# Performance work log

Hardware: AMD Instinct MI355X
Metric: run time of the kernel (lower is better)

Reference implementation:

```python
import jax, jax.numpy as jnp
import numpy as np


def _knn_graph(x, k):
    """Faithful port of DynamicLstmGnn.knn_to_graph + get_u_v, returning the
    dense symmetrized edge-weight matrix [N, N] (the original re-sparsifies
    this same matrix via coalesce; nonzero extraction is data-dependent and
    not jit-able, so the dense matrix is the canonical output)."""
    N = x.shape[0]
    # negative squared euclidean distance: -||xi||^2 + 2 xi.xj - ||xj||^2
    xx = jnp.sum(x * x, axis=1, keepdims=True)          # [N, 1]
    inner = -2.0 * (x @ x.T)                              # [N, N]
    pairwise_distance = -xx - inner - xx.T                # [N, N], <= 0
    vals, idx = jax.lax.top_k(pairwise_distance, k)       # [N, k] largest (= closest)
    rows = jnp.repeat(jnp.arange(N), k)                   # idx_prime.flatten()
    # sparse COO -> to_dense (duplicate indices sum, matching torch.sparse)
    edges = jnp.zeros((N, N), dtype=x.dtype).at[rows, idx.ravel()].add(vals.ravel())
    edges_int = (edges > 0).astype(x.dtype)
    reflected_int = edges_int + edges_int.T
    reflected_edges = edges + edges.T
    denom = jnp.where(reflected_int == 0, jnp.ones((), x.dtype), reflected_int)
    edges = reflected_edges / denom
    diag = jnp.arange(N)
    edges = edges.at[diag, diag].set(0.0)                 # fill_diagonal_(0)
    return edges


def setup_inputs() -> dict:
    key = jax.random.key(0)
    x = jax.random.normal(key, (10000, 64), dtype=jnp.float32)
    return {"x": x, "k": 5}


def reference(x, k):
    return _knn_graph(x, k)
```

## Files before the change

kernel.cpp:

```cpp
#include <hip/hip_runtime.h>

#define D 64
#define K 5
#define LK 8
#define GK 12
#define NSPLIT 16
#define NTILES 625
#define ROWBLK 157
#define NCOMP (ROWBLK * NSPLIT)
typedef unsigned int u32;
typedef unsigned long long u64;
typedef __bf16 bf16x8 __attribute__((ext_vector_type(8)));
typedef float  f32x4v __attribute__((ext_vector_type(4)));

__device__ __forceinline__ u32 med3u(u32 a, u32 b, u32 c) {
    u32 r;
    asm("v_med3_u32 %0, %1, %2, %3" : "=v"(r) : "v"(a), "v"(b), "v"(c));
    return r;
}

__device__ __forceinline__ u32 pack32(float v, int idx) {
    u32 u = __float_as_uint(v);
    u ^= ((u32)((int)u >> 31)) | 0x80000000u;
    return (u & 0xFFFFC000u) | ((~(u32)idx) & 0x3FFFu);
}
__device__ __forceinline__ int idx32(u32 key) { return (int)((~key) & 0x3FFFu); }

__device__ __forceinline__ u64 packKV(float v, int idx) {
    u32 u = __float_as_uint(v);
    u ^= ((u32)((int)u >> 31)) | 0x80000000u;
    return ((u64)u << 32) | (u32)(~idx);
}
__device__ __forceinline__ float unpackV(u64 key) {
    u32 hu = (u32)(key >> 32);
    return (hu & 0x80000000u) ? __uint_as_float(hu & 0x7fffffffu)
                              : __uint_as_float(~hu);
}

template<int LO, int LA, int LB, typename T>
__device__ __forceinline__ void mergeKeep(T a[LA], const T b[LB]) {
    T A[LA], B[LB], out[LO];
#pragma unroll
    for (int i = 0; i < LA; ++i) A[i] = a[i];
#pragma unroll
    for (int i = 0; i < LB; ++i) B[i] = b[i];
#pragma unroll
    for (int m = 0; m < LO; ++m) {
        bool ta = A[0] >= B[0];
        out[m] = ta ? A[0] : B[0];
#pragma unroll
        for (int i = 0; i < LA - 1; ++i) A[i] = ta ? A[i + 1] : A[i];
        A[LA - 1] = ta ? (T)0 : A[LA - 1];
#pragma unroll
        for (int i = 0; i < LB - 1; ++i) B[i] = ta ? B[i] : B[i + 1];
        B[LB - 1] = ta ? B[LB - 1] : (T)0;
    }
#pragma unroll
    for (int m = 0; m < LO; ++m) a[m] = out[m];
}

__global__ __launch_bounds__(256) void prep(
    const float* __restrict__ x, __bf16* __restrict__ xbA,
    float* __restrict__ xxf, float* __restrict__ xxh, int N)
{
    int g = blockIdx.x * 256 + threadIdx.x;
    const int REPACK = NTILES * 2 * 64;
    if (g < REPACK) {
        int tile = g >> 7;
        int rem  = g & 127;
        int kh   = rem >> 6;
        int lane = rem & 63;
        int q = lane >> 4, r = lane & 15;
        int row = tile * 16 + r;
        int k0  = kh * 32 + q * 8;
        const float4* p = (const float4*)(x + (size_t)row * D + k0);
        float4 v0 = p[0], v1 = p[1];
        bf16x8 o;
        o[0] = (__bf16)v0.x; o[1] = (__bf16)v0.y; o[2] = (__bf16)v0.z; o[3] = (__bf16)v0.w;
        o[4] = (__bf16)v1.x; o[5] = (__bf16)v1.y; o[6] = (__bf16)v1.z; o[7] = (__bf16)v1.w;
        ((bf16x8*)xbA)[g] = o;
        return;
    }
    int i = g - REPACK;
    if (i >= N) return;
    const float4* p = (const float4*)(x + (size_t)i * D);
    float s = 0.f;
#pragma unroll
    for (int t = 0; t < 16; ++t) {
        float4 v = p[t];
        s += v.x * v.x + v.y * v.y + v.z * v.z + v.w * v.w;
    }
    xxf[i] = s;
    xxh[i] = -0.5f * s;
}

__global__ __launch_bounds__(256) void topk_zero_mfma(
    const __bf16* __restrict__ xbA, const float* __restrict__ xxh, int N,
    u32* __restrict__ wsK, float* __restrict__ outZ, long long totalF4,
    int nZero, int f4PerZ)
{
    const int bx  = blockIdx.x;
    const int tid = threadIdx.x;
    const int g8  = bx >> 3;
    const int r8  = bx & 7;

    if (g8 % 6 == 0) {
        int zid = (g8 / 6) * 8 + r8;
        if (zid >= nZero) return;
        long long s = (long long)zid * f4PerZ;
        long long e = s + f4PerZ; if (e > totalF4) e = totalF4;
        const f32x4v z = {0.f, 0.f, 0.f, 0.f};
        for (long long i = s + tid; i < e; i += 256)
            *(f32x4v*)(outZ + 4 * i) = z;
        return;
    }

    const int cid = bx - (g8 / 6 + 1) * 8;
    if (cid >= NCOMP) return;
    const int split = cid / ROWBLK;
    const int rb    = cid - split * ROWBLK;

    const int lane = tid & 63;
    const int wave = tid >> 6;
    const int l15  = lane & 15;
    const int q    = lane >> 4;
    const int r0 = rb * 64 + wave * 16;

    const bf16x8* fb = (const bf16x8*)xbA;

    int bt = r0 >> 4; if (bt > NTILES - 1) bt = NTILES - 1;
    const bf16x8 B0 = fb[bt * 128 + lane];
    const bf16x8 B1 = fb[bt * 128 + 64 + lane];

    const bf16x8* ap = fb + (size_t)split * 128 + lane;
    const float* xhp = xxh + split * 16 + q * 4;
    u32 base16k = 0x3FFFu - (u32)(split * 16 + q * 4);
    const int apBump = NSPLIT * 128;
    const int xcBump = NSPLIT * 16;

    u32 L[LK];
#pragma unroll
    for (int m = 0; m < LK; ++m) L[m] = 0u;

    bf16x8 A0 = ap[0];
    bf16x8 A1 = ap[64];
    f32x4v xh = *(const f32x4v*)xhp;

    for (int t = split; t < NTILES; t += NSPLIT) {
        ap += apBump; xhp += xcBump;
        const bf16x8 nA0 = ap[0];
        const bf16x8 nA1 = ap[64];
        const f32x4v nxh = *(const f32x4v*)xhp;

        f32x4v acc = xh;
        acc = __builtin_amdgcn_mfma_f32_16x16x32_bf16(A0, B0, acc, 0, 0, 0);
        acc = __builtin_amdgcn_mfma_f32_16x16x32_bf16(A1, B1, acc, 0, 0, 0);

#pragma unroll
        for (int v = 0; v < 4; ++v) {
            u32 u = __float_as_uint(acc[v]);
            u ^= ((u32)((int)u >> 31)) | 0x80000000u;
            u32 key = (u & 0xFFFFC000u) | (base16k - (u32)v);
            u32 n0 = max(L[0], key);
            u32 n1 = med3u(L[0], L[1], key);
            u32 n2 = med3u(L[1], L[2], key);
            u32 n3 = med3u(L[2], L[3], key);
            u32 n4 = med3u(L[3], L[4], key);
            u32 n5 = med3u(L[4], L[5], key);
            u32 n6 = med3u(L[5], L[6], key);
            u32 n7 = med3u(L[6], L[7], key);
            L[0]=n0; L[1]=n1; L[2]=n2; L[3]=n3; L[4]=n4; L[5]=n5; L[6]=n6; L[7]=n7;
        }
        base16k -= (u32)xcBump;
        A0 = nA0; A1 = nA1; xh = nxh;
    }

#pragma unroll
    for (int mask = 16; mask <= 32; mask <<= 1) {
        u32 P[LK];
#pragma unroll
        for (int m = 0; m < LK; ++m) P[m] = (u32)__shfl_xor((int)L[m], mask);
        mergeKeep<LK, LK, LK, u32>(L, P);
    }

    if (lane < 16) {
        int row = r0 + l15;
        if (row < N) {
            u32* dst = wsK + ((size_t)row * NSPLIT + split) * LK;
#pragma unroll
            for (int m = 0; m < LK; ++m) dst[m] = L[m];
        }
    }
}

__global__ __launch_bounds__(256) void rescore_scatter(
    const u32* __restrict__ wsK, const float* __restrict__ x, const float* __restrict__ xxf,
    float* __restrict__ out, int N)
{
    const int lane = threadIdx.x & 63;
    const int wave = threadIdx.x >> 6;
    const int sub  = lane & 3;
    const int row  = blockIdx.x * 64 + wave * 16 + (lane >> 2);
    const bool vrow = (row < N);
    const int rr = vrow ? row : 0;

    u32 cur[GK];
    {
        const u32* Lp = wsK + ((size_t)rr * NSPLIT + 4 * sub) * LK;
#pragma unroll
        for (int m = 0; m < LK; ++m) cur[m] = Lp[m];
#pragma unroll
        for (int m = LK; m < GK; ++m) cur[m] = 0u;
#pragma unroll
        for (int l = 1; l < 4; ++l) {
            u32 b[LK];
#pragma unroll
            for (int m = 0; m < LK; ++m) b[m] = Lp[l * LK + m];
            mergeKeep<GK, GK, LK, u32>(cur, b);
        }
    }
#pragma unroll
    for (int mask = 1; mask <= 2; mask <<= 1) {
        u32 P[GK];
#pragma unroll
        for (int m = 0; m < GK; ++m) P[m] = (u32)__shfl_xor((int)cur[m], mask);
        mergeKeep<GK, GK, GK, u32>(cur, P);
    }

    const float nxi = xxf[rr];
    int   cj[3]; bool cval[3];
    float d[3] = {0.f, 0.f, 0.f};
    const f32x4v* pj[3];
#pragma unroll
    for (int c = 0; c < 3; ++c) {
        int j = idx32(cur[sub * 3 + c]);
        cval[c] = (j < N) && (cur[sub * 3 + c] != 0u);
        cj[c] = cval[c] ? j : 0;
        pj[c] = (const f32x4v*)(x + (size_t)cj[c] * D);
    }
    const f32x4v* xip = (const f32x4v*)(x + (size_t)rr * D);
#pragma unroll
    for (int t = 0; t < 16; ++t) {
        const f32x4v xv = xip[t];
#pragma unroll
        for (int c = 0; c < 3; ++c) {
            const f32x4v pv = pj[c][t];
            d[c] = fmaf(xv[0], pv[0], d[c]);
            d[c] = fmaf(xv[1], pv[1], d[c]);
            d[c] = fmaf(xv[2], pv[2], d[c]);
            d[c] = fmaf(xv[3], pv[3], d[c]);
        }
    }
    u64 F[K];
#pragma unroll
    for (int c = 0; c < 3; ++c) {
        float val = 2.f * d[c] - nxi - xxf[cj[c]];
        F[c] = cval[c] ? packKV(val, cj[c]) : 0ull;
    }
    F[3] = 0ull; F[4] = 0ull;
    { u64 a0=F[0],a1=F[1],a2=F[2];
      if (a0 < a1) { u64 t0=a0; a0=a1; a1=t0; }
      if (a1 < a2) { u64 t0=a1; a1=a2; a2=t0; }
      if (a0 < a1) { u64 t0=a0; a0=a1; a1=t0; }
      F[0]=a0; F[1]=a1; F[2]=a2; }
#pragma unroll
    for (int mask = 1; mask <= 2; mask <<= 1) {
        u64 P[K];
#pragma unroll
        for (int m = 0; m < K; ++m) P[m] = __shfl_xor(F[m], mask);
        mergeKeep<K, K, K, u64>(F, P);
    }

    if (sub == 0 && vrow) {
#pragma unroll
        for (int m = 0; m < K; ++m) {
            int j = (int)(~(u32)F[m]);
            if ((unsigned)j < (unsigned)N && j != row) {
                float v = unpackV(F[m]);
                atomicAdd(out + (size_t)row * N + j, v);
                atomicAdd(out + (size_t)j * N + row, v);
            }
        }
    }
}

extern "C" void kernel_launch(void* const* d_in, const int* in_sizes, int n_in,
                              void* d_out, int out_size, void* d_ws, size_t ws_size,
                              hipStream_t stream) {
    const float* x = (const float*)d_in[0];
    const int N = in_sizes[0] / D;
    float* out = (float*)d_out;

    const size_t oXB = 0;
    const size_t oXX = 0x150000;
    const size_t oXH = 0x160000;
    const size_t oWK = 0x170000;
    __bf16* xbA = (__bf16*)((char*)d_ws + oXB);
    float*  xxf = (float*)((char*)d_ws + oXX);
    float*  xxh = (float*)((char*)d_ws + oXH);
    u32*    wsK = (u32*)((char*)d_ws + oWK);

    const int prepThreads = NTILES * 2 * 64 + N;
    prep<<<(prepThreads + 255) / 256, 256, 0, stream>>>(x, xbA, xxf, xxh, N);

    long long totalF4 = (long long)out_size / 4;
    const int nBlocksTotal = 3024;
    const int nZero = 504;
    int f4PerZ = (int)((totalF4 + nZero - 1) / nZero);
    topk_zero_mfma<<<nBlocksTotal, 256, 0, stream>>>(
        xbA, xxh, N, wsK, out, totalF4, nZero, f4PerZ);

    rescore_scatter<<<ROWBLK, 256, 0, stream>>>(wsK, x, xxf, out, N);
}
```

Measured before the change: 445.2 us.

## Process four row tiles per wave to reuse streamed column fragments

Each wave now handles four 16-row tiles (64 rows) instead of one, so every column-tile fragment loaded from memory feeds four MFMA pairs and four top-k insertion chains. This cuts the global traffic per useful MFMA by roughly four and shrinks the grid from 3024 to 768 blocks, with the zero-fill block count scaled down to match. In exchange each thread holds more registers (4x top-k lists and B fragments), which may lower occupancy, and there are fewer blocks to spread across the GPU.

```diff
diff --git a/kernel.cpp b/kernel.cpp
--- a/kernel.cpp
+++ b/kernel.cpp
@@ -6,8 +6,10 @@
 #define GK 12
 #define NSPLIT 16
 #define NTILES 625
+#define RWAVE 4
+#define RBLK 40
+#define NCOMP (RBLK * NSPLIT)
 #define ROWBLK 157
-#define NCOMP (ROWBLK * NSPLIT)
 typedef unsigned int u32;
 typedef unsigned long long u64;
 typedef __bf16 bf16x8 __attribute__((ext_vector_type(8)));
@@ -19,11 +21,6 @@
     return r;
 }
 
-__device__ __forceinline__ u32 pack32(float v, int idx) {
-    u32 u = __float_as_uint(v);
-    u ^= ((u32)((int)u >> 31)) | 0x80000000u;
-    return (u & 0xFFFFC000u) | ((~(u32)idx) & 0x3FFFu);
-}
 __device__ __forceinline__ int idx32(u32 key) { return (int)((~key) & 0x3FFFu); }
 
 __device__ __forceinline__ u64 packKV(float v, int idx) {
@@ -117,20 +114,24 @@
 
     const int cid = bx - (g8 / 6 + 1) * 8;
     if (cid >= NCOMP) return;
-    const int split = cid / ROWBLK;
-    const int rb    = cid - split * ROWBLK;
+    const int split = cid / RBLK;
+    const int rb    = cid - split * RBLK;
 
     const int lane = tid & 63;
     const int wave = tid >> 6;
     const int l15  = lane & 15;
     const int q    = lane >> 4;
-    const int r0 = rb * 64 + wave * 16;
+    const int r0   = rb * 256 + wave * 64;
 
     const bf16x8* fb = (const bf16x8*)xbA;
 
-    int bt = r0 >> 4; if (bt > NTILES - 1) bt = NTILES - 1;
-    const bf16x8 B0 = fb[bt * 128 + lane];
-    const bf16x8 B1 = fb[bt * 128 + 64 + lane];
+    bf16x8 Bf[RWAVE][2];
+#pragma unroll
+    for (int l = 0; l < RWAVE; ++l) {
+        int bt = (r0 >> 4) + l; if (bt > NTILES - 1) bt = NTILES - 1;
+        Bf[l][0] = fb[bt * 128 + lane];
+        Bf[l][1] = fb[bt * 128 + 64 + lane];
+    }
 
     const bf16x8* ap = fb + (size_t)split * 128 + lane;
     const float* xhp = xxh + split * 16 + q * 4;
@@ -138,9 +139,11 @@
     const int apBump = NSPLIT * 128;
     const int xcBump = NSPLIT * 16;
 
-    u32 L[LK];
-#pragma unroll
-    for (int m = 0; m < LK; ++m) L[m] = 0u;
+    u32 L[RWAVE][LK];
+#pragma unroll
+    for (int l = 0; l < RWAVE; ++l)
+#pragma unroll
+        for (int m = 0; m < LK; ++m) L[l][m] = 0u;
 
     bf16x8 A0 = ap[0];
     bf16x8 A1 = ap[64];
@@ -152,43 +155,49 @@
         const bf16x8 nA1 = ap[64];
         const f32x4v nxh = *(const f32x4v*)xhp;
 
-        f32x4v acc = xh;
-        acc = __builtin_amdgcn_mfma_f32_16x16x32_bf16(A0, B0, acc, 0, 0, 0);
-        acc = __builtin_amdgcn_mfma_f32_16x16x32_bf16(A1, B1, acc, 0, 0, 0);
-
-#pragma unroll
-        for (int v = 0; v < 4; ++v) {
-            u32 u = __float_as_uint(acc[v]);
-            u ^= ((u32)((int)u >> 31)) | 0x80000000u;
-            u32 key = (u & 0xFFFFC000u) | (base16k - (u32)v);
-            u32 n0 = max(L[0], key);
-            u32 n1 = med3u(L[0], L[1], key);
-            u32 n2 = med3u(L[1], L[2], key);
-            u32 n3 = med3u(L[2], L[3], key);
-            u32 n4 = med3u(L[3], L[4], key);
-            u32 n5 = med3u(L[4], L[5], key);
-            u32 n6 = med3u(L[5], L[6], key);
-            u32 n7 = med3u(L[6], L[7], key);
-            L[0]=n0; L[1]=n1; L[2]=n2; L[3]=n3; L[4]=n4; L[5]=n5; L[6]=n6; L[7]=n7;
+#pragma unroll
+        for (int l = 0; l < RWAVE; ++l) {
+            f32x4v acc = xh;
+            acc = __builtin_amdgcn_mfma_f32_16x16x32_bf16(A0, Bf[l][0], acc, 0, 0, 0);
+            acc = __builtin_amdgcn_mfma_f32_16x16x32_bf16(A1, Bf[l][1], acc, 0, 0, 0);
+
+#pragma unroll
+            for (int v = 0; v < 4; ++v) {
+                u32 u = __float_as_uint(acc[v]);
+                u ^= ((u32)((int)u >> 31)) | 0x80000000u;
+                u32 key = (u & 0xFFFFC000u) | (base16k - (u32)v);
+                u32 n0 = max(L[l][0], key);
+                u32 n1 = med3u(L[l][0], L[l][1], key);
+                u32 n2 = med3u(L[l][1], L[l][2], key);
+                u32 n3 = med3u(L[l][2], L[l][3], key);
+                u32 n4 = med3u(L[l][3], L[l][4], key);
+                u32 n5 = med3u(L[l][4], L[l][5], key);
+                u32 n6 = med3u(L[l][5], L[l][6], key);
+                u32 n7 = med3u(L[l][6], L[l][7], key);
+                L[l][0]=n0; L[l][1]=n1; L[l][2]=n2; L[l][3]=n3;
+                L[l][4]=n4; L[l][5]=n5; L[l][6]=n6; L[l][7]=n7;
+            }
         }
         base16k -= (u32)xcBump;
         A0 = nA0; A1 = nA1; xh = nxh;
     }
 
 #pragma unroll
-    for (int mask = 16; mask <= 32; mask <<= 1) {
-        u32 P[LK];
-#pragma unroll
-        for (int m = 0; m < LK; ++m) P[m] = (u32)__shfl_xor((int)L[m], mask);
-        mergeKeep<LK, LK, LK, u32>(L, P);
-    }
-
-    if (lane < 16) {
-        int row = r0 + l15;
-        if (row < N) {
-            u32* dst = wsK + ((size_t)row * NSPLIT + split) * LK;
-#pragma unroll
-            for (int m = 0; m < LK; ++m) dst[m] = L[m];
+    for (int l = 0; l < RWAVE; ++l) {
+#pragma unroll
+        for (int mask = 16; mask <= 32; mask <<= 1) {
+            u32 P[LK];
+#pragma unroll
+            for (int m = 0; m < LK; ++m) P[m] = (u32)__shfl_xor((int)L[l][m], mask);
+            mergeKeep<LK, LK, LK, u32>(L[l], P);
+        }
+        if (lane < 16) {
+            int row = r0 + l * 16 + l15;
+            if (row < N) {
+                u32* dst = wsK + ((size_t)row * NSPLIT + split) * LK;
+#pragma unroll
+                for (int m = 0; m < LK; ++m) dst[m] = L[l][m];
+            }
         }
     }
 }
@@ -304,8 +313,8 @@
     prep<<<(prepThreads + 255) / 256, 256, 0, stream>>>(x, xbA, xxf, xxh, N);
 
     long long totalF4 = (long long)out_size / 4;
-    const int nBlocksTotal = 3024;
-    const int nZero = 504;
+    const int nBlocksTotal = 768;
+    const int nZero = 128;
     int f4PerZ = (int)((totalF4 + nZero - 1) / nZero);
     topk_zero_mfma<<<nBlocksTotal, 256, 0, stream>>>(
         xbA, xxh, N, wsK, out, totalF4, nZero, f4PerZ);
```

After: 430.5 us. 3.3% less time.
